# Optimization experiments

Hardware: AMD Instinct MI355X
Metric: run time of the kernel (lower is better)

The kernel has to match this reference:

```python
import jax, jax.numpy as jnp
import numpy as np
from jax import lax

N_SERIES = 1024   # embedding rows
B = 1024          # batch (= rows of Y)
T = 512           # n_time
INPUT = 28        # input_size
OUTPUT = 28       # output_size
N_T = 2           # temporal exogenous channels
N_S = 4           # static features
M = 7             # seasonality[0]


def setup_inputs() -> dict:
    key = jax.random.key(0)
    k1, k2, k3, k4, k5 = jax.random.split(key, 5)
    S = jax.random.normal(k1, (B, N_S), jnp.float32)
    # Y must be strictly positive (division + log in normalize)
    Y = jax.random.uniform(k2, (B, T), jnp.float32, 0.5, 1.5)
    X = jax.random.normal(k3, (B, N_T, T), jnp.float32)
    idxs = jax.random.randint(k4, (B,), 0, N_SERIES)
    sample_mask = jnp.ones((B, T), jnp.float32)
    # embedding table, init near 0.5 like the torch module
    embeds_weight = 0.5 + 0.05 * jax.random.normal(k5, (N_SERIES, 1 + 1 + M), jnp.float32)
    return dict(S=S, Y=Y, X=X, idxs=idxs, sample_mask=sample_mask,
                embeds_weight=embeds_weight)


def _levels_seasons(Y, embeds):
    """Single-seasonality (len(seasonality)==1) ES recurrence via lax.scan."""
    lev_sms = jax.nn.sigmoid(embeds[:, 0])      # [B]
    seas_sms = jax.nn.sigmoid(embeds[:, 1])     # [B]
    init_seas = jnp.exp(embeds[:, 2:2 + M])     # [B, M]
    s0 = init_seas[:, 0]                        # [B]
    lev0 = Y[:, 0] / s0                         # levels[0] = Y0 / seas_prod
    # seasonalities1 list = [s0..s_{M-1}, s0]; step t uses index t, so the
    # rolling buffer of the next M seasonal values starts as [s1..s_{M-1}, s0]
    buf0 = jnp.concatenate([init_seas[:, 1:], s0[:, None]], axis=1)  # [B, M]

    def step(carry, y_t):
        lev, buf = carry
        seas_t = buf[:, 0]
        newlev = lev_sms * (y_t / seas_t) + (1.0 - lev_sms) * lev
        newseas = seas_sms * (y_t / newlev) + (1.0 - seas_sms) * seas_t
        buf = jnp.concatenate([buf[:, 1:], newseas[:, None]], axis=1)
        return (newlev, buf), (newlev, newseas)

    (_, _), (levs, seass) = lax.scan(step, (lev0, buf0), Y[:, 1:].T)  # [T-1, B]
    levels = jnp.concatenate([lev0[:, None], levs.T], axis=1)         # [B, T]
    init_list = jnp.concatenate([init_seas, s0[:, None]], axis=1)     # [B, M+1]
    seasonalities = jnp.concatenate([init_list, seass.T], axis=1)     # [B, T+M]
    return levels, seasonalities


def _forward_core(S, Y, X, idxs, sample_mask, embeds_weight):
    embeds = embeds_weight[idxs]                    # embedding lookup [B, 9]
    levels, seasonalities = _levels_seasons(Y, embeds)

    W = T - INPUT - OUTPUT + 1                      # n_windows
    starts = jnp.arange(W)
    idx_in = starts[:, None] + jnp.arange(INPUT)    # [W, INPUT]

    Yw = Y[:, idx_in]                               # [B, W, INPUT]
    lev_end = levels[:, starts + INPUT - 1]         # [B, W] level at window end
    seas_in = seasonalities[:, idx_in]              # [B, W, INPUT]
    insample = jnp.log(Yw / (lev_end[:, :, None] * seas_in))  # [B, W, INPUT]

    # temporal exogenous: X[:, :, start:end+OUTPUT].reshape(B, -1)
    idx_x = starts[:, None] + jnp.arange(INPUT + OUTPUT)       # [W, I+O]
    Xw = X[:, :, idx_x]                              # [B, N_T, W, I+O]
    Xw = jnp.transpose(Xw, (0, 2, 1, 3)).reshape(Y.shape[0], W, N_T * (INPUT + OUTPUT))
    insample = jnp.concatenate([insample, Xw], axis=2)

    # static features
    Sw = jnp.broadcast_to(S[:, None, :], (Y.shape[0], W, N_S))
    insample = jnp.concatenate([insample, Sw], axis=2)          # [B, W, C]
    windows_y_insample = jnp.transpose(insample, (1, 0, 2))     # [W, B, C]

    # outsample (eval mode: raw Y, not normalized)
    idx_out = starts[:, None] + INPUT + jnp.arange(OUTPUT)      # [W, OUTPUT]
    windows_y_outsample = jnp.transpose(Y[:, idx_out], (1, 0, 2))  # [W, B, O]

    # sample_mask unfold(size=OUTPUT, step=1), keep last W windows
    n_unf = T - OUTPUT + 1
    starts_m = jnp.arange(n_unf)[-W:]
    idx_m = starts_m[:, None] + jnp.arange(OUTPUT)
    mask_w = jnp.transpose(sample_mask[:, idx_m], (1, 0, 2))    # [W, B, O]

    return windows_y_insample, windows_y_outsample, levels, seasonalities, mask_w


def reference(S, Y, X, idxs, sample_mask, embeds_weight):
    return _forward_core(S, Y, X, idxs, sample_mask, embeds_weight)
```

## Files before the change

kernel.cpp:

```cpp
#include <hip/hip_runtime.h>

#define BB   1024
#define TT   512
#define NIN  28
#define NS   4
#define MM   7
#define WW   457
#define SLEN 519
#define EMB  9

#define OUT1_SZ (WW * BB * 144)
#define OUT2_SZ (WW * BB * 28)
#define OUT3_SZ (BB * TT)
#define OUT4_SZ (BB * SLEN)

#define CH   32
#define NCH  (TT / CH)
#define NF2  (WW * BB * 7)

typedef float f4 __attribute__((ext_vector_type(4)));

__device__ __forceinline__ f4 ld4u(const float* p) {
    f4 v;
    __builtin_memcpy(&v, p, sizeof(f4));
    return v;
}

__global__ __launch_bounds__(64) void es_scan(const float* __restrict__ Y,
        const int* __restrict__ idxs, const float* __restrict__ EW,
        float* __restrict__ levels, float* __restrict__ seas) {
    __shared__ float yl[64][CH + 1];
    __shared__ float se[64][CH + 1];
    const int tid = threadIdx.x;
    const int b0  = blockIdx.x << 6;
    const int b   = b0 + tid;

    const float* e = EW + idxs[b] * EMB;
    const float lev_sms  = 1.0f / (1.0f + __expf(-e[0]));
    const float seas_sms = 1.0f / (1.0f + __expf(-e[1]));
    const float a_l = 1.0f - lev_sms;
    const float a_s = 1.0f - seas_sms;

    float buf[MM];
    const float is0 = __expf(e[2]);
    {
        float* srow = seas + b * SLEN;
        srow[0] = is0;
#pragma unroll
        for (int k = 1; k < MM; ++k) {
            float v = __expf(e[2 + k]);
            srow[k] = v;
            buf[k - 1] = v;
        }
        buf[MM - 1] = is0;
    }

    f4 pf[8];
#pragma unroll
    for (int k = 0; k < 8; ++k) {
        int flat = (k << 6) + tid;
        int r = flat >> 3, q = flat & 7;
        pf[k] = *reinterpret_cast<const f4*>(Y + (b0 + r) * TT + (q << 2));
    }

    float lev = 0.0f;

#define ES_STEP(TTI)                                                        \
    {                                                                       \
        float y  = yreg[TTI];                                               \
        float st = buf[0];                                                  \
        lev = lev_sms * __fdividef(y, st) + a_l * lev;                      \
        float ns = seas_sms * __fdividef(y, lev) + a_s * st;                \
        buf[0] = buf[1]; buf[1] = buf[2]; buf[2] = buf[3];                  \
        buf[3] = buf[4]; buf[4] = buf[5]; buf[5] = buf[6];                  \
        buf[6] = ns;                                                        \
        yl[tid][TTI] = lev;                                                 \
        se[tid][TTI] = ns;                                                  \
    }

    for (int c = 0; c < NCH; ++c) {
        __syncthreads();
#pragma unroll
        for (int k = 0; k < 8; ++k) {
            int flat = (k << 6) + tid;
            int r = flat >> 3, q = flat & 7;
            float* dst = &yl[r][q << 2];
            dst[0] = pf[k].x; dst[1] = pf[k].y; dst[2] = pf[k].z; dst[3] = pf[k].w;
        }
        __syncthreads();
        if (c < NCH - 1) {
#pragma unroll
            for (int k = 0; k < 8; ++k) {
                int flat = (k << 6) + tid;
                int r = flat >> 3, q = flat & 7;
                pf[k] = *reinterpret_cast<const f4*>(
                    Y + (b0 + r) * TT + (c + 1) * CH + (q << 2));
            }
        }

        float yreg[CH];
#pragma unroll
        for (int tt = 0; tt < CH; ++tt) yreg[tt] = yl[tid][tt];

        if (c == 0) {
            lev = __fdividef(yreg[0], is0);
            yl[tid][0] = lev;
            se[tid][0] = is0;
#pragma unroll
            for (int tt = 1; tt < CH; ++tt) ES_STEP(tt)
        } else {
#pragma unroll
            for (int tt = 0; tt < CH; ++tt) ES_STEP(tt)
        }
        __syncthreads();

#pragma unroll
        for (int k = 0; k < CH; ++k) {
            int flat = (k << 6) + tid;
            int r    = flat >> 5;
            int col  = flat & 31;
            levels[(b0 + r) * TT   + c * CH + col]      = yl[r][col];
            seas  [(b0 + r) * SLEN + MM + c * CH + col] = se[r][col];
        }
    }
#undef ES_STEP
}

#define LYSo 0
#define LYSs 273
#define XSo  546
#define XSs  293
#define LLo  1718
#define LLs  237
#define SSo  2192
#define ZRo  2200
#define ULEN 2201
#define OST  (7 * 1024 * 36)

__device__ __forceinline__ void tload(int i, int g0, int b0,
        const float* __restrict__ Y, const float* __restrict__ seas,
        const float* __restrict__ X, const float* __restrict__ levels,
        f4& a, f4& b) {
    if (i < 128) {
        int bl = i >> 6, k = i & 63, t = g0 + (k << 2);
        a = ld4u(Y    + (b0 + bl) * TT   + t);
        b = ld4u(seas + (b0 + bl) * SLEN + t);
    } else if (i < 412) {
        int j = i - 128, blc = j / 71, k = j - blc * 71;
        int t = g0 + (k << 2); if (t > 508) t = 508;
        a = ld4u(X + (size_t)((b0 + (blc >> 1)) * 2 + (blc & 1)) * TT + t);
    } else if (i < 528) {
        int j = i - 412, bl = j / 58, k = j - bl * 58;
        a = ld4u(levels + (b0 + bl) * TT + g0 + 24 + (k << 2));
    }
}

__device__ __forceinline__ void twrite(int i, int g0, float* U, f4 a, f4 b) {
    if (i < 128) {
        int bl = i >> 6, k = i & 63, base = LYSo + bl * LYSs + (k << 2);
        U[base + 0] = __logf(a.x) - __logf(b.x);
        U[base + 1] = __logf(a.y) - __logf(b.y);
        U[base + 2] = __logf(a.z) - __logf(b.z);
        U[base + 3] = __logf(a.w) - __logf(b.w);
    } else if (i < 412) {
        int j = i - 128, blc = j / 71, k = j - blc * 71;
        int wb = (k << 2); if (g0 + wb > 508) wb = 508 - g0;
        int base = XSo + blc * XSs + wb;
        U[base + 0] = a.x; U[base + 1] = a.y;
        U[base + 2] = a.z; U[base + 3] = a.w;
    } else if (i < 528) {
        int j = i - 412, bl = j / 58, k = j - bl * 58;
        int base = LLo + bl * LLs + (k << 2);
        U[base + 0] = __logf(a.x); U[base + 1] = __logf(a.y);
        U[base + 2] = __logf(a.z); U[base + 3] = __logf(a.w);
    }
}

__device__ __forceinline__ void tstore(int tid, int g0, int NW, int b0,
        const float* U, f4* __restrict__ out1) {
    if (tid >= 504) return;
    int go  = tid / 72;
    int r   = tid - go * 72;
    int bl  = (r >= 36) ? 1 : 0;
    int col = r - 36 * bl;
    int pa, la, dp, dl;
    if (col < 7) {
        pa = LYSo + bl * LYSs + go + (col << 2);
        la = LLo  + bl * LLs  + go + 3;
        dp = 7; dl = 7;
    } else if (col < 35) {
        int ch = (col >= 21) ? 1 : 0;
        int jj = col - 7 - 14 * ch;
        pa = XSo + ((bl << 1) | ch) * XSs + go + (jj << 2);
        la = ZRo; dp = 7; dl = 0;
    } else {
        pa = SSo + (bl << 2);
        la = ZRo; dp = 0; dl = 0;
    }
    int off = (((g0 + go) << 10) + b0 + bl) * 36 + col;
#define ST1 { float l = U[la]; f4 v;                                        \
    v.x = U[pa] - l; v.y = U[pa + 1] - l;                                   \
    v.z = U[pa + 2] - l; v.w = U[pa + 3] - l;                               \
    __builtin_nontemporal_store(v, out1 + off);                             \
    pa += dp; la += dl; off += OST; }
#pragma unroll 4
    for (int t = 0; t < 32; ++t) ST1
    if (go + 224 < NW) ST1
#undef ST1
}

__global__ __launch_bounds__(512) void k_out1(const float* __restrict__ Y,
        const float* __restrict__ X, const float* __restrict__ S,
        const float* __restrict__ levels, const float* __restrict__ seas,
        f4* __restrict__ out1) {
    __shared__ float U[ULEN];
    const int tid = threadIdx.x;
    const int b0  = (int)blockIdx.x << 1;

    f4 a, b, e, eb, a2, b2, e2, eb2, sv;

    tload(tid, 0, b0, Y, seas, X, levels, a, b);
    if (tid < 16) tload(512 + tid, 0, b0, Y, seas, X, levels, e, eb);
    if (tid < 2)  sv = *reinterpret_cast<const f4*>(S + ((b0 + tid) << 2));

    twrite(tid, 0, U, a, b);
    if (tid < 16) twrite(512 + tid, 0, U, e, eb);
    if (tid < 2) {
        int base = SSo + (tid << 2);
        U[base] = sv.x; U[base + 1] = sv.y; U[base + 2] = sv.z; U[base + 3] = sv.w;
    }
    if (tid == 2) U[ZRo] = 0.0f;
    __syncthreads();

    tload(tid, 229, b0, Y, seas, X, levels, a2, b2);
    if (tid < 16) tload(512 + tid, 229, b0, Y, seas, X, levels, e2, eb2);

    tstore(tid, 0, 229, b0, U, out1);
    __syncthreads();

    twrite(tid, 229, U, a2, b2);
    if (tid < 16) twrite(512 + tid, 229, U, e2, eb2);
    __syncthreads();

    tstore(tid, 229, 228, b0, U, out1);
}

__global__ __launch_bounds__(256) void k_out25(const float* __restrict__ Y,
        const float* __restrict__ mask, f4* __restrict__ out2,
        f4* __restrict__ out5) {
    int i = blockIdx.x * blockDim.x + threadIdx.x;
    const int stride = gridDim.x * blockDim.x;
    for (; i < NF2; i += stride) {
        int wb = i / 7;
        int j  = i - wb * 7;
        int b  = wb & (BB - 1);
        int w  = wb >> 10;
        int base = w + NIN + (j << 2);
        f4 vy = ld4u(Y    + b * TT + base);
        f4 vm = ld4u(mask + b * TT + base);
        __builtin_nontemporal_store(vy, &out2[i]);
        __builtin_nontemporal_store(vm, &out5[i]);
    }
}

extern "C" void kernel_launch(void* const* d_in, const int* in_sizes, int n_in,
                              void* d_out, int out_size, void* d_ws, size_t ws_size,
                              hipStream_t stream) {
    const float* S    = (const float*)d_in[0];
    const float* Y    = (const float*)d_in[1];
    const float* X    = (const float*)d_in[2];
    const int*   idxs = (const int*)d_in[3];
    const float* mask = (const float*)d_in[4];
    const float* EW   = (const float*)d_in[5];

    float* out  = (float*)d_out;
    float* out1 = out;
    float* out2 = out1 + OUT1_SZ;
    float* out3 = out2 + OUT2_SZ;
    float* out4 = out3 + OUT3_SZ;
    float* out5 = out4 + OUT4_SZ;

    es_scan<<<16, 64, 0, stream>>>(Y, idxs, EW, out3, out4);
    k_out1<<<512, 512, 0, stream>>>(Y, X, S, out3, out4, (f4*)out1);
    k_out25<<<2048, 256, 0, stream>>>(Y, mask, (f4*)out2, (f4*)out5);
}
```

Measured before the change: 126.3 us.

## Fuse ES scan with out2/out5 copy kernel to overlap serial scan

Merges the serial exponential-smoothing scan and the independent window-copy kernel into one launch. The first 16 blocks run the scan, with 256 threads sharing the Y staging and global writeback while only 64 threads do the recurrence. The remaining 2048 blocks perform the out2/out5 copy. The aim is to hide the long latency-bound scan behind the bandwidth-bound copy and save a launch, at the cost of wider scan blocks with idle lanes during the recurrence.

```diff
diff --git a/kernel.cpp b/kernel.cpp
--- a/kernel.cpp
+++ b/kernel.cpp
@@ -26,44 +26,49 @@
     return v;
 }
 
-__global__ __launch_bounds__(64) void es_scan(const float* __restrict__ Y,
-        const int* __restrict__ idxs, const float* __restrict__ EW,
-        float* __restrict__ levels, float* __restrict__ seas) {
+__global__ __launch_bounds__(256, 8) void k_scan_out25(
+        const float* __restrict__ Y, const int* __restrict__ idxs,
+        const float* __restrict__ EW, const float* __restrict__ mask,
+        float* __restrict__ levels, float* __restrict__ seas,
+        f4* __restrict__ out2, f4* __restrict__ out5) {
     __shared__ float yl[64][CH + 1];
     __shared__ float se[64][CH + 1];
+
     const int tid = threadIdx.x;
-    const int b0  = blockIdx.x << 6;
-    const int b   = b0 + tid;
-
-    const float* e = EW + idxs[b] * EMB;
-    const float lev_sms  = 1.0f / (1.0f + __expf(-e[0]));
-    const float seas_sms = 1.0f / (1.0f + __expf(-e[1]));
-    const float a_l = 1.0f - lev_sms;
-    const float a_s = 1.0f - seas_sms;
-
-    float buf[MM];
-    const float is0 = __expf(e[2]);
-    {
-        float* srow = seas + b * SLEN;
-        srow[0] = is0;
-#pragma unroll
-        for (int k = 1; k < MM; ++k) {
-            float v = __expf(e[2 + k]);
-            srow[k] = v;
-            buf[k - 1] = v;
-        }
-        buf[MM - 1] = is0;
-    }
-
-    f4 pf[8];
-#pragma unroll
-    for (int k = 0; k < 8; ++k) {
-        int flat = (k << 6) + tid;
-        int r = flat >> 3, q = flat & 7;
-        pf[k] = *reinterpret_cast<const f4*>(Y + (b0 + r) * TT + (q << 2));
-    }
-
-    float lev = 0.0f;
+
+    if (blockIdx.x < 16) {
+        const int b0 = blockIdx.x << 6;
+        const int bs = b0 + (tid & 63);
+
+        const float* e = EW + idxs[bs] * EMB;
+        const float lev_sms  = 1.0f / (1.0f + __expf(-e[0]));
+        const float seas_sms = 1.0f / (1.0f + __expf(-e[1]));
+        const float a_l = 1.0f - lev_sms;
+        const float a_s = 1.0f - seas_sms;
+
+        float buf[MM];
+        const float is0 = __expf(e[2]);
+        {
+            float* srow = seas + bs * SLEN;
+            if (tid < 64) srow[0] = is0;
+#pragma unroll
+            for (int k = 1; k < MM; ++k) {
+                float v = __expf(e[2 + k]);
+                if (tid < 64) srow[k] = v;
+                buf[k - 1] = v;
+            }
+            buf[MM - 1] = is0;
+        }
+
+        f4 pf[2];
+#pragma unroll
+        for (int k = 0; k < 2; ++k) {
+            int flat = (k << 8) + tid;
+            int r = flat >> 3, q = flat & 7;
+            pf[k] = *reinterpret_cast<const f4*>(Y + (b0 + r) * TT + (q << 2));
+        }
+
+        float lev = 0.0f;
 
 #define ES_STEP(TTI)                                                        \
     {                                                                       \
@@ -78,52 +83,69 @@
         se[tid][TTI] = ns;                                                  \
     }
 
-    for (int c = 0; c < NCH; ++c) {
-        __syncthreads();
-#pragma unroll
-        for (int k = 0; k < 8; ++k) {
-            int flat = (k << 6) + tid;
-            int r = flat >> 3, q = flat & 7;
-            float* dst = &yl[r][q << 2];
-            dst[0] = pf[k].x; dst[1] = pf[k].y; dst[2] = pf[k].z; dst[3] = pf[k].w;
-        }
-        __syncthreads();
-        if (c < NCH - 1) {
+        for (int c = 0; c < NCH; ++c) {
+            __syncthreads();
+#pragma unroll
+            for (int k = 0; k < 2; ++k) {
+                int flat = (k << 8) + tid;
+                int r = flat >> 3, q = flat & 7;
+                float* dst = &yl[r][q << 2];
+                dst[0] = pf[k].x; dst[1] = pf[k].y;
+                dst[2] = pf[k].z; dst[3] = pf[k].w;
+            }
+            __syncthreads();
+            if (c < NCH - 1) {
+#pragma unroll
+                for (int k = 0; k < 2; ++k) {
+                    int flat = (k << 8) + tid;
+                    int r = flat >> 3, q = flat & 7;
+                    pf[k] = *reinterpret_cast<const f4*>(
+                        Y + (b0 + r) * TT + (c + 1) * CH + (q << 2));
+                }
+            }
+
+            if (tid < 64) {
+                float yreg[CH];
+#pragma unroll
+                for (int tt = 0; tt < CH; ++tt) yreg[tt] = yl[tid][tt];
+
+                if (c == 0) {
+                    lev = __fdividef(yreg[0], is0);
+                    yl[tid][0] = lev;
+                    se[tid][0] = is0;
+#pragma unroll
+                    for (int tt = 1; tt < CH; ++tt) ES_STEP(tt)
+                } else {
+#pragma unroll
+                    for (int tt = 0; tt < CH; ++tt) ES_STEP(tt)
+                }
+            }
+            __syncthreads();
+
 #pragma unroll
             for (int k = 0; k < 8; ++k) {
-                int flat = (k << 6) + tid;
-                int r = flat >> 3, q = flat & 7;
-                pf[k] = *reinterpret_cast<const f4*>(
-                    Y + (b0 + r) * TT + (c + 1) * CH + (q << 2));
-            }
-        }
-
-        float yreg[CH];
-#pragma unroll
-        for (int tt = 0; tt < CH; ++tt) yreg[tt] = yl[tid][tt];
-
-        if (c == 0) {
-            lev = __fdividef(yreg[0], is0);
-            yl[tid][0] = lev;
-            se[tid][0] = is0;
-#pragma unroll
-            for (int tt = 1; tt < CH; ++tt) ES_STEP(tt)
-        } else {
-#pragma unroll
-            for (int tt = 0; tt < CH; ++tt) ES_STEP(tt)
-        }
-        __syncthreads();
-
-#pragma unroll
-        for (int k = 0; k < CH; ++k) {
-            int flat = (k << 6) + tid;
-            int r    = flat >> 5;
-            int col  = flat & 31;
-            levels[(b0 + r) * TT   + c * CH + col]      = yl[r][col];
-            seas  [(b0 + r) * SLEN + MM + c * CH + col] = se[r][col];
-        }
-    }
+                int flat = (k << 8) + tid;
+                int r    = flat >> 5;
+                int col  = flat & 31;
+                levels[(b0 + r) * TT   + c * CH + col]      = yl[r][col];
+                seas  [(b0 + r) * SLEN + MM + c * CH + col] = se[r][col];
+            }
+        }
 #undef ES_STEP
+    } else {
+        const int id = blockIdx.x - 16;
+        for (int i = (id << 8) + tid; i < NF2; i += 2048 * 256) {
+            int wb = i / 7;
+            int j  = i - wb * 7;
+            int b  = wb & (BB - 1);
+            int w  = wb >> 10;
+            int base = w + NIN + (j << 2);
+            f4 vy = ld4u(Y    + b * TT + base);
+            f4 vm = ld4u(mask + b * TT + base);
+            __builtin_nontemporal_store(vy, &out2[i]);
+            __builtin_nontemporal_store(vm, &out5[i]);
+        }
+    }
 }
 
 #define LYSo 0
@@ -245,24 +267,6 @@
     tstore(tid, 229, 228, b0, U, out1);
 }
 
-__global__ __launch_bounds__(256) void k_out25(const float* __restrict__ Y,
-        const float* __restrict__ mask, f4* __restrict__ out2,
-        f4* __restrict__ out5) {
-    int i = blockIdx.x * blockDim.x + threadIdx.x;
-    const int stride = gridDim.x * blockDim.x;
-    for (; i < NF2; i += stride) {
-        int wb = i / 7;
-        int j  = i - wb * 7;
-        int b  = wb & (BB - 1);
-        int w  = wb >> 10;
-        int base = w + NIN + (j << 2);
-        f4 vy = ld4u(Y    + b * TT + base);
-        f4 vm = ld4u(mask + b * TT + base);
-        __builtin_nontemporal_store(vy, &out2[i]);
-        __builtin_nontemporal_store(vm, &out5[i]);
-    }
-}
-
 extern "C" void kernel_launch(void* const* d_in, const int* in_sizes, int n_in,
                               void* d_out, int out_size, void* d_ws, size_t ws_size,
                               hipStream_t stream) {
@@ -280,7 +284,7 @@
     float* out4 = out3 + OUT3_SZ;
     float* out5 = out4 + OUT4_SZ;
 
-    es_scan<<<16, 64, 0, stream>>>(Y, idxs, EW, out3, out4);
+    k_scan_out25<<<2064, 256, 0, stream>>>(Y, idxs, EW, mask, out3, out4,
+                                           (f4*)out2, (f4*)out5);
     k_out1<<<512, 512, 0, stream>>>(Y, X, S, out3, out4, (f4*)out1);
-    k_out25<<<2048, 256, 0, stream>>>(Y, mask, (f4*)out2, (f4*)out5);
-}
+}
```

Measured after the change: 149.9 us. 18.7% more time.
